# Performance work log

Hardware: AMD Instinct MI355X
Metric: run time of the kernel (lower is better)

Reference implementation:

```python
import jax, jax.numpy as jnp
import numpy as np

N = 65536          # nodes
E = 1048576        # edges (avg degree 16)
K = 5              # B-spline kernel size per dim (dim=3 -> 125 kernels)
F_IN, F_OUT = 1, 32
GRID = 32          # first sparse_voxel_max_pool: size = 1/32 -> 32^3 voxels
NUM_VOX = GRID ** 3

# enumerate the 2^3 corners of the degree-1 B-spline support
_BITS = np.array([[(b >> d) & 1 for d in range(3)] for b in range(8)], dtype=np.int32)  # [8,3]
_STRIDES = np.array([1, K, K * K], dtype=np.int32)  # kernel index strides per dim


def setup_inputs() -> dict:
    key = jax.random.key(0)
    ks = jax.random.split(key, 7)
    x = jax.random.normal(ks[0], (N, F_IN), dtype=jnp.float32)
    edge_index = jax.random.randint(ks[1], (2, E), 0, N, dtype=jnp.int32)
    pseudo = jax.random.uniform(ks[2], (E, 3), dtype=jnp.float32)   # edge pseudo-coords in [0,1]^3
    pos = jax.random.uniform(ks[3], (N, 3), dtype=jnp.float32)      # node positions in [0,1]^3
    W = jax.random.normal(ks[4], (K ** 3, F_IN, F_OUT), dtype=jnp.float32) * 0.1
    W_root = jax.random.normal(ks[5], (F_IN, F_OUT), dtype=jnp.float32) * 0.1
    bias = jax.random.normal(ks[6], (F_OUT,), dtype=jnp.float32) * 0.1
    return {"x": x, "edge_index": edge_index, "pseudo": pseudo, "pos": pos,
            "W": W, "W_root": W_root, "bias": bias}


def spline_basis(pseudo):
    """Degree-1 open B-spline basis. Returns (weights [E,8], kernel_idx [E,8])."""
    v = pseudo * (K - 1)                                   # [E,3] in [0, K-1]
    i0 = jnp.clip(jnp.floor(v), 0, K - 2)                  # lower knot per dim
    f = v - i0                                             # fractional part
    i0 = i0.astype(jnp.int32)
    bits = jnp.asarray(_BITS)                              # [8,3]
    idx = i0[:, None, :] + bits[None]                      # [E,8,3]
    w = jnp.where(bits[None].astype(bool), f[:, None, :], 1.0 - f[:, None, :])
    B = w.prod(axis=-1)                                    # [E,8]
    kidx = (idx * jnp.asarray(_STRIDES)).sum(axis=-1)      # [E,8] in [0,125)
    return B, kidx


def spline_conv(x, edge_index, pseudo, W, W_root, bias):
    src, dst = edge_index[0], edge_index[1]
    B, kidx = spline_basis(pseudo)                         # [E,8], [E,8]
    xj = x[src]                                            # [E,F_IN] edge-wise gather
    Wg = W[kidx]                                           # [E,8,F_IN,F_OUT]
    msg = jnp.einsum('es,ef,esfo->eo', B, xj, Wg)          # basis-weighted messages [E,F_OUT]
    agg = jax.ops.segment_sum(msg, dst, num_segments=N)    # scatter-add
    deg = jax.ops.segment_sum(jnp.ones((E,), jnp.float32), dst, num_segments=N)
    out = agg / jnp.clip(deg, 1.0)[:, None] + x @ W_root + bias  # mean aggr + root + bias
    return out


def reference(x, edge_index, pseudo, pos, W, W_root, bias):
    h = jax.nn.elu(spline_conv(x, edge_index, pseudo, W, W_root, bias))  # [N,32]
    # sparse voxel max pooling: hash positions to a 32^3 grid, scatter-max features
    vid = jnp.clip(jnp.floor(pos * GRID), 0, GRID - 1).astype(jnp.int32)  # [N,3]
    vidx = vid[:, 0] + GRID * vid[:, 1] + GRID * GRID * vid[:, 2]         # [N]
    pooled = jax.ops.segment_max(h, vidx, num_segments=NUM_VOX)           # [32768,32]
    pooled = jnp.where(jnp.isfinite(pooled), pooled, 0.0)                 # empty voxels -> 0
    return pooled
```

## Files before the change

### kernel.cpp

```cpp
#include <hip/hip_runtime.h>
#include <math.h>

#define F_OUT     32
#define GRID_DIM  32
#define NUM_VOX   (GRID_DIM * GRID_DIM * GRID_DIM)

#define NPB   64
#define NBKT  1024
#define SEB   2048
#define SCS   132
#define DEGS  125
#define ECAP  3072

__device__ __forceinline__ unsigned int enc_f32(float f) {
    unsigned int u = __float_as_uint(f);
    return (u & 0x80000000u) ? ~u : (u | 0x80000000u);
}
__device__ __forceinline__ float dec_f32(unsigned int e) {
    return (e & 0x80000000u) ? __uint_as_float(e ^ 0x80000000u)
                             : __uint_as_float(~e);
}

__global__ __launch_bounds__(512) void sort_kernel(
    const int*   __restrict__ src,
    const int*   __restrict__ dst,
    const float* __restrict__ x,
    const float* __restrict__ pseudo,
    float4* __restrict__ payload,
    unsigned int* __restrict__ off_tab,
    int E)
{
    __shared__ unsigned int sHist[NBKT];
    __shared__ unsigned int sStart[NBKT];
    __shared__ unsigned int sScan[512];
    __shared__ __align__(16) float4 sPay[SEB];

    const int t  = threadIdx.x;
    const int e0 = blockIdx.x * SEB;

    for (int i = t; i < NBKT; i += 512) sHist[i] = 0;
    __syncthreads();

    unsigned short dloc[4];
    float4 pay[4];
    #pragma unroll
    for (int i = 0; i < 4; ++i) {
        int e = e0 + i * 512 + t;
        if (e < E) {
            int d = dst[e];
            int s = src[e];
            float p0 = pseudo[3 * e], p1 = pseudo[3 * e + 1], p2 = pseudo[3 * e + 2];
            float xj = x[s];
            unsigned int q2 = (unsigned int)(p2 * 65535.0f + 0.5f) & 0xFFFFu;
            unsigned int w  = q2 | ((unsigned int)(d & 63) << 16);
            dloc[i] = (unsigned short)d;
            pay[i]  = make_float4(p0, p1, xj, __uint_as_float(w));
            atomicAdd(&sHist[d >> 6], 1u);
        } else dloc[i] = 0;
    }
    __syncthreads();

    unsigned int a0 = sHist[2 * t], a1 = sHist[2 * t + 1];
    sScan[t] = a0 + a1;
    __syncthreads();
    for (int ofs = 1; ofs < 512; ofs <<= 1) {
        unsigned int v = (t >= ofs) ? sScan[t - ofs] : 0u;
        __syncthreads();
        sScan[t] += v;
        __syncthreads();
    }
    unsigned int excl = sScan[t] - (a0 + a1);
    sStart[2 * t]     = excl;
    sStart[2 * t + 1] = excl + a0;
    __syncthreads();
    sHist[2 * t]     = excl;
    sHist[2 * t + 1] = excl + a0;
    __syncthreads();
    const unsigned int total = sScan[511];

    #pragma unroll
    for (int i = 0; i < 4; ++i) {
        int e = e0 + i * 512 + t;
        if (e < E) {
            unsigned int slot = atomicAdd(&sHist[dloc[i] >> 6], 1u);
            sPay[slot] = pay[i];
        }
    }
    __syncthreads();

    for (unsigned int i = t; i < total; i += 512)
        payload[(size_t)e0 + i] = sPay[i];

    for (int b = t; b < NBKT; b += 512) {
        unsigned int s = sStart[b];
        unsigned int nxt = (b < NBKT - 1) ? sStart[b + 1] : total;
        off_tab[(size_t)blockIdx.x * NBKT + b] = s | ((nxt - s) << 16);
    }
}

__device__ __forceinline__ void process_edge(float4 r, float* sC)
{
    float xj = r.z;
    unsigned int w = __float_as_uint(r.w);
    int   rel = (int)((w >> 16) & 63u);
    float p2  = (float)(w & 0xFFFFu) * (1.0f / 65535.0f);

    float v0 = r.x * 4.0f, v1 = r.y * 4.0f, v2 = p2 * 4.0f;
    float i0 = fminf(fmaxf(floorf(v0), 0.0f), 3.0f);
    float i1 = fminf(fmaxf(floorf(v1), 0.0f), 3.0f);
    float i2 = fminf(fmaxf(floorf(v2), 0.0f), 3.0f);
    float f0 = v0 - i0, f1 = v1 - i1, f2 = v2 - i2;
    float g0 = 1.0f - f0, g1 = 1.0f - f1, g2 = 1.0f - f2;
    int k = (int)i0 + 5 * (int)i1 + 25 * (int)i2;

    float w00 = g0 * g1, w10 = f0 * g1, w01 = g0 * f1, w11 = f0 * f1;
    float a2 = xj * g2, b2 = xj * f2;
    float* row = sC + rel * SCS;
    atomicAdd(row + k +  0, w00 * a2);
    atomicAdd(row + k +  1, w10 * a2);
    atomicAdd(row + k +  5, w01 * a2);
    atomicAdd(row + k +  6, w11 * a2);
    atomicAdd(row + k + 25, w00 * b2);
    atomicAdd(row + k + 26, w10 * b2);
    atomicAdd(row + k + 30, w01 * b2);
    atomicAdd(row + k + 31, w11 * b2);
    atomicAdd(row + DEGS, 1.0f);
}

__global__ __launch_bounds__(512) void owner_kernel(
    const float4* __restrict__ payload,
    const unsigned int* __restrict__ off_tab,
    const float* __restrict__ W,
    const float* __restrict__ x,
    const float* __restrict__ W_root,
    const float* __restrict__ bias,
    const float* __restrict__ pos,
    unsigned int* __restrict__ pooled,
    int Nn, int nSB)
{
    __shared__ __align__(16) float sC[NPB * SCS];
    __shared__ unsigned int sEdge[ECAP];
    __shared__ unsigned int sNe;

    const int t = threadIdx.x;
    const int b = blockIdx.x;
    const int lane = t & 63;

    for (int i = t; i < NPB * SCS / 4; i += 512)
        *(float4*)&sC[i * 4] = make_float4(0.f, 0.f, 0.f, 0.f);
    if (t == 0) sNe = 0;

    unsigned int cnt = 0, start_g = 0;
    if (t < nSB) {
        unsigned int packed = off_tab[(size_t)t * NBKT + b];
        start_g = (unsigned int)t * SEB + (packed & 0xFFFFu);
        cnt = packed >> 16;
    }
    __syncthreads();

    unsigned int incl = cnt;
    #pragma unroll
    for (int d = 1; d < 64; d <<= 1) {
        unsigned int v = __shfl_up(incl, d, 64);
        if (lane >= d) incl += v;
    }
    unsigned int wtot = __shfl(incl, 63, 64);
    unsigned int wbase = 0;
    if (lane == 63 && wtot > 0) wbase = atomicAdd(&sNe, wtot);
    wbase = __shfl(wbase, 63, 64);
    unsigned int off = wbase + incl - cnt;

    for (unsigned int j = 0; j < cnt; ++j) {
        unsigned int p = off + j;
        if (p < ECAP) sEdge[p] = start_g + j;
        else process_edge(payload[start_g + j], sC);
    }
    __syncthreads();

    int ne = (int)sNe; if (ne > ECAP) ne = ECAP;
    for (int i = t; i < ne; i += 512)
        process_edge(payload[sEdge[i]], sC);
    __syncthreads();

    const int node = t & 63;
    const int cg   = t >> 6;
    const float* crow = sC + node * SCS;
    float4 acc = make_float4(0.f, 0.f, 0.f, 0.f);
    #pragma unroll 8
    for (int k4 = 0; k4 < 31; ++k4) {
        float4 r = *(const float4*)&crow[k4 * 4];
        const float* wp = W + (k4 * 4) * F_OUT + cg * 4;
        float4 w0 = *(const float4*)(wp);
        float4 w1 = *(const float4*)(wp + F_OUT);
        float4 w2 = *(const float4*)(wp + 2 * F_OUT);
        float4 w3 = *(const float4*)(wp + 3 * F_OUT);
        acc.x += r.x * w0.x + r.y * w1.x + r.z * w2.x + r.w * w3.x;
        acc.y += r.x * w0.y + r.y * w1.y + r.z * w2.y + r.w * w3.y;
        acc.z += r.x * w0.z + r.y * w1.z + r.z * w2.z + r.w * w3.z;
        acc.w += r.x * w0.w + r.y * w1.w + r.z * w2.w + r.w * w3.w;
    }
    {
        float r = crow[124];
        const float* wp = W + 124 * F_OUT + cg * 4;
        acc.x += r * wp[0]; acc.y += r * wp[1];
        acc.z += r * wp[2]; acc.w += r * wp[3];
    }
    float dg = fmaxf(crow[DEGS], 1.0f);
    int   n  = b * NPB + node;
    float xn = (n < Nn) ? x[n] : 0.0f;
    float4 wr = *(const float4*)(W_root + cg * 4);
    float4 bs = *(const float4*)(bias + cg * 4);
    __syncthreads();

    if (n < Nn) {
        float h;
        h = acc.x / dg + xn * wr.x + bs.x; h = h > 0.f ? h : expm1f(h); sC[node * SCS + cg * 4 + 0] = h;
        h = acc.y / dg + xn * wr.y + bs.y; h = h > 0.f ? h : expm1f(h); sC[node * SCS + cg * 4 + 1] = h;
        h = acc.z / dg + xn * wr.z + bs.z; h = h > 0.f ? h : expm1f(h); sC[node * SCS + cg * 4 + 2] = h;
        h = acc.w / dg + xn * wr.w + bs.w; h = h > 0.f ? h : expm1f(h); sC[node * SCS + cg * 4 + 3] = h;
    }
    __syncthreads();

    for (int item = t; item < NPB * F_OUT; item += 512) {
        int nr = item >> 5, o = item & 31;
        int nn = b * NPB + nr;
        if (nn >= Nn) break;
        int vx = min(max((int)floorf(pos[3 * nn + 0] * (float)GRID_DIM), 0), GRID_DIM - 1);
        int vy = min(max((int)floorf(pos[3 * nn + 1] * (float)GRID_DIM), 0), GRID_DIM - 1);
        int vz = min(max((int)floorf(pos[3 * nn + 2] * (float)GRID_DIM), 0), GRID_DIM - 1);
        int vidx = vx + GRID_DIM * vy + GRID_DIM * GRID_DIM * vz;
        atomicMax(&pooled[(size_t)vidx * F_OUT + o], enc_f32(sC[nr * SCS + o]));
    }
}

__global__ __launch_bounds__(256) void finalize_kernel(
    const unsigned int* __restrict__ pooled,
    float* __restrict__ out, int M)
{
    int i = blockIdx.x * blockDim.x + threadIdx.x;
    if (i >= M) return;
    unsigned int u = pooled[i];
    out[i] = (u == 0u) ? 0.0f : dec_f32(u);
}

extern "C" void kernel_launch(void* const* d_in, const int* in_sizes, int n_in,
                              void* d_out, int out_size, void* d_ws, size_t ws_size,
                              hipStream_t stream) {
    const float* x       = (const float*)d_in[0];
    const int*   ei      = (const int*)  d_in[1];
    const float* pseudo  = (const float*)d_in[2];
    const float* pos     = (const float*)d_in[3];
    const float* W       = (const float*)d_in[4];
    const float* W_root  = (const float*)d_in[5];
    const float* bias    = (const float*)d_in[6];
    float* out = (float*)d_out;

    const int E   = in_sizes[1] / 2;
    const int Nn  = in_sizes[0];
    const int nSB = (E + SEB - 1) / SEB;
    const int nb  = (Nn + NPB - 1) / NPB;

    const size_t pooled_b = (size_t)NUM_VOX * F_OUT * 4;
    const size_t off_b    = (size_t)nSB * NBKT * 4;
    unsigned int* pooled  = (unsigned int*)d_ws;
    unsigned int* off_tab = (unsigned int*)((char*)d_ws + pooled_b);
    float4*       payload = (float4*)((char*)d_ws + pooled_b + ((off_b + 15) & ~(size_t)15));

    hipMemsetAsync(pooled, 0, pooled_b, stream);

    sort_kernel<<<nSB, 512, 0, stream>>>(ei, ei + E, x, pseudo, payload, off_tab, E);
    owner_kernel<<<nb, 512, 0, stream>>>(payload, off_tab, W, x, W_root, bias, pos,
                                         pooled, Nn, nSB);

    const int M = (out_size < NUM_VOX * F_OUT) ? out_size : NUM_VOX * F_OUT;
    finalize_kernel<<<(M + 255) / 256, 256, 0, stream>>>(pooled, out, M);
}
```

Measured before the change: 167.3 us.

## Use wave-shuffle scan in sort and split voxel max-pool into separate kernel

The sort kernel's block-wide Hillis-Steele scan through shared memory with many barriers is replaced by a per-wave shuffle scan plus a small cross-wave total, and the kernel gets a launch-bounds occupancy hint. The owner kernel no longer does the voxel atomicMax tail. It writes the per-node activations to a workspace buffer, and a new voxmax kernel does the scatter-max with one thread per node-feature. This shortens the owner kernel's serial tail and the sort barriers, at the cost of an extra launch and a round trip of the activations through global memory.

```diff
diff --git a/kernel.cpp b/kernel.cpp
--- a/kernel.cpp
+++ b/kernel.cpp
@@ -21,7 +21,7 @@
                              : __uint_as_float(~e);
 }
 
-__global__ __launch_bounds__(512) void sort_kernel(
+__global__ __launch_bounds__(512, 4) void sort_kernel(
     const int*   __restrict__ src,
     const int*   __restrict__ dst,
     const float* __restrict__ x,
@@ -32,11 +32,13 @@
 {
     __shared__ unsigned int sHist[NBKT];
     __shared__ unsigned int sStart[NBKT];
-    __shared__ unsigned int sScan[512];
+    __shared__ unsigned int sWTot[8];
     __shared__ __align__(16) float4 sPay[SEB];
 
-    const int t  = threadIdx.x;
-    const int e0 = blockIdx.x * SEB;
+    const int t    = threadIdx.x;
+    const int lane = t & 63;
+    const int wv   = t >> 6;
+    const int e0   = blockIdx.x * SEB;
 
     for (int i = t; i < NBKT; i += 512) sHist[i] = 0;
     __syncthreads();
@@ -61,22 +63,28 @@
     __syncthreads();
 
     unsigned int a0 = sHist[2 * t], a1 = sHist[2 * t + 1];
-    sScan[t] = a0 + a1;
-    __syncthreads();
-    for (int ofs = 1; ofs < 512; ofs <<= 1) {
-        unsigned int v = (t >= ofs) ? sScan[t - ofs] : 0u;
-        __syncthreads();
-        sScan[t] += v;
-        __syncthreads();
-    }
-    unsigned int excl = sScan[t] - (a0 + a1);
-    sStart[2 * t]     = excl;
-    sStart[2 * t + 1] = excl + a0;
-    __syncthreads();
-    sHist[2 * t]     = excl;
-    sHist[2 * t + 1] = excl + a0;
-    __syncthreads();
-    const unsigned int total = sScan[511];
+    unsigned int pairSum = a0 + a1;
+    unsigned int incl = pairSum;
+    #pragma unroll
+    for (int d = 1; d < 64; d <<= 1) {
+        unsigned int v = __shfl_up(incl, d, 64);
+        if (lane >= d) incl += v;
+    }
+    if (lane == 63) sWTot[wv] = incl;
+    __syncthreads();
+    unsigned int wofs = 0, total = 0;
+    #pragma unroll
+    for (int w = 0; w < 8; ++w) {
+        unsigned int v = sWTot[w];
+        if (w < wv) wofs += v;
+        total += v;
+    }
+    unsigned int ex = wofs + incl - pairSum;
+    sStart[2 * t]     = ex;
+    sStart[2 * t + 1] = ex + a0;
+    sHist[2 * t]      = ex;
+    sHist[2 * t + 1]  = ex + a0;
+    __syncthreads();
 
     #pragma unroll
     for (int i = 0; i < 4; ++i) {
@@ -134,8 +142,7 @@
     const float* __restrict__ x,
     const float* __restrict__ W_root,
     const float* __restrict__ bias,
-    const float* __restrict__ pos,
-    unsigned int* __restrict__ pooled,
+    float4* __restrict__ h4,
     int Nn, int nSB)
 {
     __shared__ __align__(16) float sC[NPB * SCS];
@@ -221,16 +228,29 @@
     }
     __syncthreads();
 
-    for (int item = t; item < NPB * F_OUT; item += 512) {
-        int nr = item >> 5, o = item & 31;
-        int nn = b * NPB + nr;
-        if (nn >= Nn) break;
-        int vx = min(max((int)floorf(pos[3 * nn + 0] * (float)GRID_DIM), 0), GRID_DIM - 1);
-        int vy = min(max((int)floorf(pos[3 * nn + 1] * (float)GRID_DIM), 0), GRID_DIM - 1);
-        int vz = min(max((int)floorf(pos[3 * nn + 2] * (float)GRID_DIM), 0), GRID_DIM - 1);
-        int vidx = vx + GRID_DIM * vy + GRID_DIM * GRID_DIM * vz;
-        atomicMax(&pooled[(size_t)vidx * F_OUT + o], enc_f32(sC[nr * SCS + o]));
-    }
+    const int n0 = b * NPB;
+    for (int item = t; item < NPB * 8; item += 512) {
+        int nr = item >> 3, q = item & 7;
+        if (n0 + nr >= Nn) break;
+        h4[(size_t)n0 * 8 + item] = *(const float4*)&sC[nr * SCS + q * 4];
+    }
+}
+
+__global__ __launch_bounds__(256) void voxmax_kernel(
+    const float* __restrict__ h,
+    const float* __restrict__ pos,
+    unsigned int* __restrict__ pooled,
+    int Nn)
+{
+    int gid = blockIdx.x * 256 + threadIdx.x;
+    int n = gid >> 5, o = gid & 31;
+    if (n >= Nn) return;
+    float hv = h[(size_t)n * F_OUT + o];
+    int vx = min(max((int)floorf(pos[3 * n + 0] * (float)GRID_DIM), 0), GRID_DIM - 1);
+    int vy = min(max((int)floorf(pos[3 * n + 1] * (float)GRID_DIM), 0), GRID_DIM - 1);
+    int vz = min(max((int)floorf(pos[3 * n + 2] * (float)GRID_DIM), 0), GRID_DIM - 1);
+    int vidx = vx + GRID_DIM * vy + GRID_DIM * GRID_DIM * vz;
+    atomicMax(&pooled[(size_t)vidx * F_OUT + o], enc_f32(hv));
 }
 
 __global__ __launch_bounds__(256) void finalize_kernel(
@@ -261,16 +281,20 @@
     const int nb  = (Nn + NPB - 1) / NPB;
 
     const size_t pooled_b = (size_t)NUM_VOX * F_OUT * 4;
-    const size_t off_b    = (size_t)nSB * NBKT * 4;
+    const size_t off_b    = ((size_t)nSB * NBKT * 4 + 15) & ~(size_t)15;
+    const size_t pay_b    = (size_t)nSB * SEB * 16;
     unsigned int* pooled  = (unsigned int*)d_ws;
     unsigned int* off_tab = (unsigned int*)((char*)d_ws + pooled_b);
-    float4*       payload = (float4*)((char*)d_ws + pooled_b + ((off_b + 15) & ~(size_t)15));
+    float4*       payload = (float4*)((char*)d_ws + pooled_b + off_b);
+    float4*       h4      = (float4*)((char*)d_ws + pooled_b + off_b + pay_b);
 
     hipMemsetAsync(pooled, 0, pooled_b, stream);
 
     sort_kernel<<<nSB, 512, 0, stream>>>(ei, ei + E, x, pseudo, payload, off_tab, E);
-    owner_kernel<<<nb, 512, 0, stream>>>(payload, off_tab, W, x, W_root, bias, pos,
-                                         pooled, Nn, nSB);
+    owner_kernel<<<nb, 512, 0, stream>>>(payload, off_tab, W, x, W_root, bias,
+                                         h4, Nn, nSB);
+    voxmax_kernel<<<(Nn * F_OUT + 255) / 256, 256, 0, stream>>>(
+        (const float*)h4, pos, pooled, Nn);
 
     const int M = (out_size < NUM_VOX * F_OUT) ? out_size : NUM_VOX * F_OUT;
     finalize_kernel<<<(M + 255) / 256, 256, 0, stream>>>(pooled, out, M);
```

After: 175.1 us. 1.05x slower.
